# Optimization experiments

Hardware: AMD Instinct MI355X
Metric: run time of the kernel (lower is better)

## Reference

```python
import jax, jax.numpy as jnp
import numpy as np
import math

B, IMG, P, C_IN = 32, 32, 2, 4
D, TED, L, H = 768, 256, 12, 12
GRID = IMG // P            # 16
N = GRID * GRID            # 256 patches
HD = D // H                # 64 head dim
MLP_H = 4 * D
RPD = 2 * GRID - 1         # 31 relative-position table side


def _ln(x, w, b, eps=1e-6):
    m = x.mean(-1, keepdims=True)
    v = ((x - m) ** 2).mean(-1, keepdims=True)
    return (x - m) * jax.lax.rsqrt(v + eps) * w + b


def _rel_idx():
    c = jnp.arange(GRID)
    ch, cw = jnp.meshgrid(c, c, indexing='ij')
    cf = jnp.stack([ch.reshape(-1), cw.reshape(-1)])          # [2, N]
    rel = cf[:, :, None] - cf[:, None, :] + (GRID - 1)        # [2, N, N] in [0, 2*GRID-2]
    return rel[0], rel[1]


def setup_inputs() -> dict:
    key = jax.random.key(0)
    ks = iter(jax.random.split(key, 64))
    def nrm(shape, s=0.02):
        return jax.random.normal(next(ks), shape, jnp.float32) * s
    z = lambda *s: jnp.zeros(s, jnp.float32)
    o = lambda *s: jnp.ones(s, jnp.float32)
    return dict(
        x=jax.random.normal(next(ks), (B, C_IN, IMG, IMG), jnp.float32),
        t=jax.random.uniform(next(ks), (B,), jnp.float32) * 1000.0,
        patch_w=nrm((D, C_IN, P, P), 0.5), patch_b=z(D),
        pos_embed=nrm((1, N, D)),
        t_w1=nrm((TED, D)), t_b1=z(D), t_w2=nrm((D, D)), t_b2=z(D),
        norm1_w=o(L, D), norm1_b=z(L, D),
        wqs=nrm((L, D, D)), bqs=z(L, D), wqt=nrm((L, D, D)), bqt=z(L, D),
        wks=nrm((L, D, D)), bks=z(L, D), wkt=nrm((L, D, D)), bkt=z(L, D),
        wvs=nrm((L, D, D)), bvs=z(L, D), wvt=nrm((L, D, D)), bvt=z(L, D),
        attn_proj_w=nrm((L, D, D)), attn_proj_b=z(L, D),
        rpb=nrm((L, RPD, RPD, H)),
        norm2_w=o(L, D), norm2_b=z(L, D),
        mlp_w1=nrm((L, D, MLP_H)), mlp_b1=z(L, MLP_H),
        mlp_w2=nrm((L, MLP_H, D)), mlp_b2=z(L, D),
        norm_w=o(D), norm_b=z(D),
        dec_w=nrm((D, P * P * C_IN)), dec_b=z(P * P * C_IN),
    )


def reference(x, t, patch_w, patch_b, pos_embed, t_w1, t_b1, t_w2, t_b2,
              norm1_w, norm1_b, wqs, bqs, wqt, bqt, wks, bks, wkt, bkt,
              wvs, bvs, wvt, bvt, attn_proj_w, attn_proj_b, rpb,
              norm2_w, norm2_b, mlp_w1, mlp_b1, mlp_w2, mlp_b2,
              norm_w, norm_b, dec_w, dec_b):
    Bn = x.shape[0]
    # patch embed: stride==kernel Conv2d as reshape + einsum -> [B, N, D]
    xr = x.reshape(Bn, C_IN, GRID, P, GRID, P)
    x_s = jnp.einsum('bcipjq,ecpq->bije', xr, patch_w).reshape(Bn, N, D) + patch_b
    x_s = x_s + pos_embed
    # sinusoidal time embedding + MLP -> [B, D]
    half = TED // 2
    freq = jnp.exp(jnp.arange(half, dtype=jnp.float32) * (-math.log(10000.0) / (half - 1)))
    emb = t[:, None] * freq[None, :]
    emb = jnp.concatenate([jnp.sin(emb), jnp.cos(emb)], axis=-1)
    x_t = jax.nn.silu(emb @ t_w1 + t_b1) @ t_w2 + t_b2
    ih, iw = _rel_idx()
    scale = HD ** -0.5
    for l in range(L):
        h = _ln(x_s, norm1_w[l], norm1_b[l])
        q = h @ wqs[l] + bqs[l] + (x_t @ wqt[l] + bqt[l])[:, None, :]
        k = h @ wks[l] + bks[l] + (x_t @ wkt[l] + bkt[l])[:, None, :]
        v = h @ wvs[l] + bvs[l] + (x_t @ wvt[l] + bvt[l])[:, None, :]
        q = q.reshape(Bn, N, H, HD)
        k = k.reshape(Bn, N, H, HD)
        v = v.reshape(Bn, N, H, HD)
        bias = rpb[l][ih, iw]                                  # gather: [N, N, H]
        attn = jnp.einsum('bnhd,bmhd->bhnm', q, k) * scale + bias.transpose(2, 0, 1)[None]
        attn = jax.nn.softmax(attn, axis=-1)
        o_ = jnp.einsum('bhnm,bmhd->bnhd', attn, v).reshape(Bn, N, D)
        x_s = x_s + (o_ @ attn_proj_w[l] + attn_proj_b[l])
        h2 = _ln(x_s, norm2_w[l], norm2_b[l])
        x_s = x_s + (jax.nn.silu(h2 @ mlp_w1[l] + mlp_b1[l]) @ mlp_w2[l] + mlp_b2[l])
    x_s = _ln(x_s, norm_w, norm_b)
    x_s = x_s @ dec_w + dec_b                                  # [B, N, P*P*C]
    # unpatchify -> [B, C, IMG, IMG]
    xo = x_s.reshape(Bn, GRID, GRID, C_IN, P, P).transpose(0, 3, 1, 4, 2, 5)
    return xo.reshape(Bn, C_IN, GRID * P, GRID * P)
```

## Files before the change

kernel.cpp:

```cpp
#include <hip/hip_runtime.h>
#include <hip/hip_bf16.h>

typedef __attribute__((ext_vector_type(8))) short short8;
typedef __attribute__((ext_vector_type(4))) short s16x4;
typedef __attribute__((ext_vector_type(4))) float f32x4;
typedef __hip_bfloat16 bf16;

#define AS1 __attribute__((address_space(1)))
#define AS3 __attribute__((address_space(3)))

__device__ __forceinline__ float b2f(short u) {
  union { unsigned int i; float f; } x;
  x.i = ((unsigned int)(unsigned short)u) << 16;
  return x.f;
}
__device__ __forceinline__ short f2bs(float f) {
  bf16 t = __float2bfloat16(f);
  return *reinterpret_cast<short*>(&t);
}

__device__ __forceinline__ void gld_lds16(const void* g, void* lds) {
  __builtin_amdgcn_global_load_lds((const AS1 unsigned int*)g,
                                   (AS3 unsigned int*)lds, 16, 0, 0);
}

__global__ void transpose_conv(const float* __restrict__ src, bf16* __restrict__ dst,
                               int R, int C, int row_off, long long layer_stride) {
  __shared__ float t[32][33];
  int l = blockIdx.z;
  int r0 = blockIdx.y * 32;
  int c0 = blockIdx.x * 32;
  int tx = threadIdx.x & 31, ty = threadIdx.x >> 5;
  const float* s = src + (size_t)l * R * C;
#pragma unroll
  for (int i = 0; i < 4; ++i)
    t[ty + i * 8][tx] = s[(size_t)(r0 + ty + i * 8) * C + c0 + tx];
  __syncthreads();
  bf16* d = dst + (size_t)l * layer_stride;
#pragma unroll
  for (int i = 0; i < 4; ++i) {
    int n = c0 + ty + i * 8, k = r0 + tx;
    d[(size_t)(row_off + n) * R + k] = __float2bfloat16(t[tx][ty + i * 8]);
  }
}

__global__ void dec_transpose(const float* __restrict__ dw, bf16* __restrict__ dwT) {
  int idx = blockIdx.x * 256 + threadIdx.x;
  if (idx >= 12288) return;
  int k = idx % 768, j = idx / 768;
  dwT[j * 768 + k] = __float2bfloat16(dw[k * 16 + j]);
}

__global__ void patch_embed(const float* __restrict__ x, const float* __restrict__ pw,
                            const float* __restrict__ pb, const float* __restrict__ pos,
                            float* __restrict__ xs) {
  int idx = blockIdx.x * 256 + threadIdx.x;
  int d = idx % 768;
  int n = (idx / 768) & 255;
  int b = idx / (768 * 256);
  int gi = n >> 4, gj = n & 15;
  float acc = pb[d];
#pragma unroll
  for (int c = 0; c < 4; ++c)
#pragma unroll
    for (int p = 0; p < 2; ++p)
#pragma unroll
      for (int q = 0; q < 2; ++q)
        acc += x[((b * 4 + c) * 32 + gi * 2 + p) * 32 + gj * 2 + q] *
               pw[((d * 4 + c) * 2 + p) * 2 + q];
  xs[idx] = acc + pos[n * 768 + d];
}

__global__ void temb_kernel(const float* __restrict__ t, float* __restrict__ emb) {
  int b = blockIdx.x;
  int i = threadIdx.x;
  float f = __expf((float)i * (-logf(10000.f) / 127.f));
  float e = t[b] * f;
  emb[b * 256 + i] = sinf(e);
  emb[b * 256 + 128 + i] = cosf(e);
}

template <int MODE>
__global__ void smallmm_red(const float* __restrict__ in, const float* __restrict__ w,
                            const float* __restrict__ bias, void* __restrict__ out, int K) {
  int tid = threadIdx.x;
  int s = tid & 7, o = blockIdx.x * 32 + (tid >> 3);
  int d = o % 768, b = o / 768;
  int Ks = K >> 3, k0 = s * Ks;
  const float* ir = in + b * K + k0;
  const float* wr = w + (size_t)k0 * 768 + d;
  float a = 0.f;
  for (int i = 0; i < Ks; ++i) a += ir[i] * wr[(size_t)i * 768];
  a += __shfl_xor(a, 1);
  a += __shfl_xor(a, 2);
  a += __shfl_xor(a, 4);
  if (s == 0) {
    a += bias[d];
    if (MODE == 0) {
      a = a / (1.f + __expf(-a));
      ((float*)out)[o] = a;
    } else {
      ((bf16*)out)[o] = __float2bfloat16(a);
    }
  }
}

__global__ void build_btab_frag(const float* __restrict__ rpb, bf16* __restrict__ btf) {
  int idx = blockIdx.x * 256 + threadIdx.x;
  int t = idx & 65535;
  int lh = idx >> 16;
  int h = lh % 12, l = lh / 12;
  int r = t & 3; t >>= 2;
  int lane = t & 63; t >>= 6;
  int i = t & 3; t >>= 2;
  int w = t & 3; t >>= 2;
  int jb = t & 1; t >>= 1;
  int hc = t & 7;
  int q = w * 64 + i * 16 + (lane & 15);
  int k = hc * 32 + jb * 16 + (lane >> 4) * 4 + r;
  int ih = (q >> 4) - (k >> 4) + 15;
  int iw = (q & 15) - (k & 15) + 15;
  btf[idx] = __float2bfloat16(8.0f * rpb[((l * 31 + ih) * 31 + iw) * 12 + h]);
}

__global__ __launch_bounds__(256) void ln_bf16_kernel(const float* __restrict__ x,
                                                      const float* __restrict__ w,
                                                      const float* __restrict__ b,
                                                      bf16* __restrict__ out) {
  int row = blockIdx.x * 4 + (threadIdx.x >> 6);
  int lane = threadIdx.x & 63;
  const float* xr = x + (size_t)row * 768;
  float v[12];
  float s = 0.f, s2 = 0.f;
#pragma unroll
  for (int k = 0; k < 12; ++k) {
    v[k] = xr[lane + k * 64];
    s += v[k];
    s2 += v[k] * v[k];
  }
#pragma unroll
  for (int off = 32; off; off >>= 1) {
    s += __shfl_xor(s, off);
    s2 += __shfl_xor(s2, off);
  }
  float m = s * (1.f / 768.f);
  float var = s2 * (1.f / 768.f) - m * m;
  float r = rsqrtf(var + 1e-6f);
  bf16* orow = out + (size_t)row * 768;
#pragma unroll
  for (int k = 0; k < 12; ++k) {
    int c = lane + k * 64;
    orow[c] = __float2bfloat16((v[k] - m) * r * w[c] + b[c]);
  }
}

template <int EPI>
__global__ __launch_bounds__(256) void gemm128(
    const bf16* __restrict__ A, int lda, const bf16* __restrict__ BT, int ldb, int K,
    const float* __restrict__ p0, const float* __restrict__ p1,
    const float* __restrict__ p2, const float* __restrict__ p3,
    const float* __restrict__ p4, const float* __restrict__ p5,
    const float* __restrict__ resid, float* __restrict__ outF,
    bf16* __restrict__ outB, int ldc) {
  __shared__ __align__(16) char lds[49152];
  const int tid = threadIdx.x;
  const int wid = tid >> 6, lane = tid & 63;
  const int wr = wid >> 1, wc = wid & 1;
  const int nwg = gridDim.x * gridDim.y;
  const int bid = blockIdx.y * gridDim.x + blockIdx.x;
  const int swzb = (bid & 7) * (nwg >> 3) + (bid >> 3);
  const int m0 = (swzb / gridDim.x) * 128, n0 = (swzb % gridDim.x) * 128;
  const int l16 = lane & 15, lq = lane >> 4;

  f32x4 acc[4][4];
#pragma unroll
  for (int i = 0; i < 4; ++i)
#pragma unroll
    for (int j = 0; j < 4; ++j) acc[i][j] = f32x4{0.f, 0.f, 0.f, 0.f};

  const int arow = tid >> 2;
  const int aslot = (tid & 3) ^ ((tid >> 4) & 3);
  const bf16* gA = A + (size_t)(m0 + arow) * lda + aslot * 8;
  const bf16* gB = BT + (size_t)(n0 + arow) * ldb + aslot * 8;
  const unsigned offw = (unsigned)__builtin_amdgcn_readfirstlane((tid & ~63) * 16);

  const int NT = K >> 5;
  auto stage = [&](int t, int buf) {
    char* pA = lds + buf * 16384;
    char* pB = pA + 8192;
    const int k = t * 32;
#pragma unroll
    for (int e = 0; e < 2; ++e) {
      gld_lds16(gA + (size_t)(e * 64) * lda + k, pA + e * 4096 + offw);
      gld_lds16(gB + (size_t)(e * 64) * ldb + k, pB + e * 4096 + offw);
    }
  };

  stage(0, 0);
  if (NT > 1) stage(1, 1);
  int cb = 0;
  for (int t = 0; t < NT; ++t) {
    if (t + 2 < NT) {
      int sb = cb + 2; if (sb >= 3) sb -= 3;
      stage(t + 2, sb);
      asm volatile("s_waitcnt vmcnt(8)" ::: "memory");
    } else if (t + 1 < NT) {
      asm volatile("s_waitcnt vmcnt(4)" ::: "memory");
    } else {
      asm volatile("s_waitcnt vmcnt(0)" ::: "memory");
    }
    __builtin_amdgcn_s_barrier();
    char* pA = lds + cb * 16384;
    char* pB = pA + 8192;
    short8 af[4], bfr[4];
    const unsigned ko = ((unsigned)(lq * 16)) ^ ((unsigned)(l16 >> 2) << 4);
#pragma unroll
    for (int i = 0; i < 4; ++i) {
      af[i]  = *(const short8*)(pA + (wr * 64 + i * 16 + l16) * 64 + ko);
      bfr[i] = *(const short8*)(pB + (wc * 64 + i * 16 + l16) * 64 + ko);
    }
#pragma unroll
    for (int i = 0; i < 4; ++i)
#pragma unroll
      for (int j = 0; j < 4; ++j)
        acc[i][j] = __builtin_amdgcn_mfma_f32_16x16x32_bf16(af[i], bfr[j], acc[i][j], 0, 0, 0);
    __builtin_amdgcn_s_barrier();
    cb = (cb == 2) ? 0 : cb + 1;
  }

#pragma unroll
  for (int i = 0; i < 4; ++i) {
#pragma unroll
    for (int j = 0; j < 4; ++j) {
#pragma unroll
      for (int r = 0; r < 4; ++r) {
        int row = m0 + wr * 64 + i * 16 + lq * 4 + r;
        int col = n0 + wc * 64 + j * 16 + l16;
        float v = acc[i][j][r];
        if constexpr (EPI == 0) {
          int s = col / 768, d = col % 768;
          int b = row >> 8;
          const float* bs = (s == 0) ? p0 : (s == 1) ? p1 : p2;
          const float* ts = (s == 0) ? p3 : (s == 1) ? p4 : p5;
          v += bs[d] + ts[b * 768 + d];
          outB[(size_t)row * ldc + col] = __float2bfloat16(v);
        } else if constexpr (EPI == 1) {
          v += p0[col] + resid[(size_t)row * ldc + col];
          outF[(size_t)row * ldc + col] = v;
        } else if constexpr (EPI == 2) {
          v += p0[col];
          v = v / (1.f + __expf(-v));
          outB[(size_t)row * ldc + col] = __float2bfloat16(v);
        } else if constexpr (EPI == 3) {
          if (row < 32) {
            int l = col / 2304;
            int r2c = col - l * 2304;
            int s = r2c / 768, d = r2c - s * 768;
            const float* bs = (s == 0) ? p0 : (s == 1) ? p1 : p2;
            v += bs[l * 768 + d];
            outF[(size_t)((l * 3 + s) * 32 + row) * 768 + d] = v;
          }
        } else {
          if (col < 16) {
            v += p0[col];
            int b = row >> 8, n = row & 255;
            int gi = n >> 4, gj = n & 15;
            int c = col >> 2, pp = (col >> 1) & 1, qq = col & 1;
            outF[((b * 4 + c) * 32 + gi * 2 + pp) * 32 + gj * 2 + qq] = v;
          }
        }
      }
    }
  }
}

__global__ __launch_bounds__(256) void attn_mfma(const bf16* __restrict__ qkv,
                                                 const bf16* __restrict__ btf,
                                                 bf16* __restrict__ obuf) {
  __shared__ __align__(16) char lds[65536];
  const int tid = threadIdx.x;
  const int wave = tid >> 6, lane = tid & 63;
  const int l16 = lane & 15, lq = lane >> 4;
  const int b = blockIdx.x / 12, h = blockIdx.x % 12;
  const bf16* qb = qkv + (size_t)b * 256 * 2304;

  {
    const short8* vrow = (const short8*)(qb + (size_t)tid * 2304 + 1536 + h * 64);
    short8 vv[8];
#pragma unroll
    for (int c = 0; c < 8; ++c) vv[c] = vrow[c];
#pragma unroll
    for (int c = 0; c < 8; ++c)
#pragma unroll
      for (int e = 0; e < 8; ++e) {
        int d = c * 8 + e;
        unsigned off = (unsigned)(d * 512 + tid * 2) ^ ((unsigned)(d & 7) << 4);
        *(short*)(lds + off) = vv[c][e];
      }
  }
  short8 qf[4][2];
#pragma unroll
  for (int i = 0; i < 4; ++i)
#pragma unroll
    for (int ks = 0; ks < 2; ++ks)
      qf[i][ks] = *(const short8*)(qb + (size_t)(wave * 64 + i * 16 + l16) * 2304 +
                                   h * 64 + ks * 32 + lq * 8);
  __syncthreads();

  f32x4 oacc[4][4];
#pragma unroll
  for (int i = 0; i < 4; ++i)
#pragma unroll
    for (int j = 0; j < 4; ++j) oacc[i][j] = f32x4{0.f, 0.f, 0.f, 0.f};
  float lp[4] = {0.f, 0.f, 0.f, 0.f};
  const bf16* bl = btf + (size_t)h * 65536 + lane * 4;
  const unsigned swzv = ((unsigned)(l16 & 7)) << 4;
  const unsigned swzp = ((unsigned)(l16 & 3)) << 4;

  for (int hc = 0; hc < 8; ++hc) {
    short8 kf[2][2];
#pragma unroll
    for (int jb = 0; jb < 2; ++jb) {
      const bf16* kr = qb + (size_t)(hc * 32 + jb * 16 + l16) * 2304 + 768 + h * 64 + lq * 8;
      kf[jb][0] = *(const short8*)(kr);
      kf[jb][1] = *(const short8*)(kr + 32);
    }
    f32x4 sacc[4][2];
#pragma unroll
    for (int i = 0; i < 4; ++i)
#pragma unroll
      for (int jb = 0; jb < 2; ++jb) {
        s16x4 bv = *(const s16x4*)(bl + ((size_t)((hc * 2 + jb) * 16 + wave * 4 + i) << 8));
        sacc[i][jb] = f32x4{b2f(bv[0]), b2f(bv[1]), b2f(bv[2]), b2f(bv[3])};
      }
#pragma unroll
    for (int jb = 0; jb < 2; ++jb)
#pragma unroll
      for (int i = 0; i < 4; ++i) {
        sacc[i][jb] = __builtin_amdgcn_mfma_f32_16x16x32_bf16(kf[jb][0], qf[i][0], sacc[i][jb], 0, 0, 0);
        sacc[i][jb] = __builtin_amdgcn_mfma_f32_16x16x32_bf16(kf[jb][1], qf[i][1], sacc[i][jb], 0, 0, 0);
      }
    char* Pw = lds + 32768 + (hc & 1) * 16384 + wave * 4096;
#pragma unroll
    for (int i = 0; i < 4; ++i)
#pragma unroll
      for (int jb = 0; jb < 2; ++jb) {
        float p0 = __expf(sacc[i][jb][0] * 0.125f);
        float p1 = __expf(sacc[i][jb][1] * 0.125f);
        float p2 = __expf(sacc[i][jb][2] * 0.125f);
        float p3 = __expf(sacc[i][jb][3] * 0.125f);
        lp[i] += (p0 + p1) + (p2 + p3);
        s16x4 pk = {f2bs(p0), f2bs(p1), f2bs(p2), f2bs(p3)};
        *(s16x4*)(Pw + (i * 16 + l16) * 64 + (((unsigned)(jb * 32 + lq * 8)) ^ swzp)) = pk;
      }
    asm volatile("s_waitcnt lgkmcnt(0)" ::: "memory");
    __builtin_amdgcn_sched_barrier(0);
    short8 pa[4], vb[4];
#pragma unroll
    for (int i = 0; i < 4; ++i)
      pa[i] = *(const short8*)(Pw + (i * 16 + l16) * 64 + (((unsigned)(lq * 16)) ^ swzp));
#pragma unroll
    for (int dj = 0; dj < 4; ++dj)
      vb[dj] = *(const short8*)(lds + (dj * 16 + l16) * 512 +
                                (((unsigned)(hc * 64 + lq * 16)) ^ swzv));
#pragma unroll
    for (int i = 0; i < 4; ++i)
#pragma unroll
      for (int dj = 0; dj < 4; ++dj)
        oacc[i][dj] = __builtin_amdgcn_mfma_f32_16x16x32_bf16(pa[i], vb[dj], oacc[i][dj], 0, 0, 0);
  }

#pragma unroll
  for (int i = 0; i < 4; ++i) {
    float l = lp[i];
    l += __shfl_xor(l, 16);
    l += __shfl_xor(l, 32);
#pragma unroll
    for (int r = 0; r < 4; ++r) {
      float linv = 1.f / __shfl(l, lq * 4 + r);
      int grow = b * 256 + wave * 64 + i * 16 + lq * 4 + r;
#pragma unroll
      for (int dj = 0; dj < 4; ++dj)
        obuf[(size_t)grow * 768 + h * 64 + dj * 16 + l16] =
            __float2bfloat16(oacc[i][dj][r] * linv);
    }
  }
}

extern "C" void kernel_launch(void* const* d_in, const int* in_sizes, int n_in,
                              void* d_out, int out_size, void* d_ws, size_t ws_size,
                              hipStream_t stream) {
  (void)in_sizes; (void)n_in; (void)out_size; (void)ws_size;
  const float* x       = (const float*)d_in[0];
  const float* t_in    = (const float*)d_in[1];
  const float* patch_w = (const float*)d_in[2];
  const float* patch_b = (const float*)d_in[3];
  const float* pos     = (const float*)d_in[4];
  const float* t_w1    = (const float*)d_in[5];
  const float* t_b1    = (const float*)d_in[6];
  const float* t_w2    = (const float*)d_in[7];
  const float* t_b2    = (const float*)d_in[8];
  const float* norm1_w = (const float*)d_in[9];
  const float* norm1_b = (const float*)d_in[10];
  const float* wqs     = (const float*)d_in[11];
  const float* bqs     = (const float*)d_in[12];
  const float* wqt     = (const float*)d_in[13];
  const float* bqt     = (const float*)d_in[14];
  const float* wks     = (const float*)d_in[15];
  const float* bks     = (const float*)d_in[16];
  const float* wkt     = (const float*)d_in[17];
  const float* bkt     = (const float*)d_in[18];
  const float* wvs     = (const float*)d_in[19];
  const float* bvs     = (const float*)d_in[20];
  const float* wvt     = (const float*)d_in[21];
  const float* bvt     = (const float*)d_in[22];
  const float* projw   = (const float*)d_in[23];
  const float* projb   = (const float*)d_in[24];
  const float* rpb     = (const float*)d_in[25];
  const float* norm2_w = (const float*)d_in[26];
  const float* norm2_b = (const float*)d_in[27];
  const float* mlp_w1  = (const float*)d_in[28];
  const float* mlp_b1  = (const float*)d_in[29];
  const float* mlp_w2  = (const float*)d_in[30];
  const float* mlp_b2  = (const float*)d_in[31];
  const float* norm_w  = (const float*)d_in[32];
  const float* norm_b  = (const float*)d_in[33];
  const float* dec_w   = (const float*)d_in[34];
  const float* dec_b   = (const float*)d_in[35];

  char* ws = (char*)d_ws;
  size_t off = 0;
  auto alloc = [&](size_t bytes) -> void* {
    void* p = ws + off;
    off += (bytes + 255) & ~(size_t)255;
    return p;
  };
  bf16* wqkvT = (bf16*)alloc(12ull * 2304 * 768 * 2);
  bf16* projT = (bf16*)alloc(12ull * 768 * 768 * 2);
  bf16* mlp1T = (bf16*)alloc(12ull * 3072 * 768 * 2);
  bf16* mlp2T = (bf16*)alloc(12ull * 768 * 3072 * 2);
  bf16* wtT   = (bf16*)alloc(12ull * 2304 * 768 * 2);
  float* xs   = (float*)alloc(8192ull * 768 * 4);
  bf16* hbuf  = (bf16*)alloc(8192ull * 768 * 2);
  bf16* qkvb  = (bf16*)alloc(8192ull * 2304 * 2);
  bf16* obuf  = (bf16*)alloc(8192ull * 768 * 2);
  bf16* btabf = (bf16*)alloc(12ull * 12 * 256 * 256 * 2);
  float* ttok = (float*)alloc(12ull * 3 * 32 * 768 * 4);
  bf16* xtb   = (bf16*)alloc(128ull * 768 * 2);
  bf16* dwT   = (bf16*)alloc(128ull * 768 * 2);
  float* emb  = (float*)alloc(32ull * 256 * 4);
  float* h1   = (float*)alloc(32ull * 768 * 4);
  bf16* hmlp  = qkvb;

  hipMemsetAsync(xtb, 0, 128ull * 768 * 2, stream);
  hipMemsetAsync(dwT, 0, 128ull * 768 * 2, stream);

  transpose_conv<<<dim3(24, 24, 12), 256, 0, stream>>>(wqs, wqkvT, 768, 768, 0, 2304ll * 768);
  transpose_conv<<<dim3(24, 24, 12), 256, 0, stream>>>(wks, wqkvT, 768, 768, 768, 2304ll * 768);
  transpose_conv<<<dim3(24, 24, 12), 256, 0, stream>>>(wvs, wqkvT, 768, 768, 1536, 2304ll * 768);
  transpose_conv<<<dim3(24, 24, 12), 256, 0, stream>>>(projw, projT, 768, 768, 0, 768ll * 768);
  transpose_conv<<<dim3(96, 24, 12), 256, 0, stream>>>(mlp_w1, mlp1T, 768, 3072, 0, 3072ll * 768);
  transpose_conv<<<dim3(24, 96, 12), 256, 0, stream>>>(mlp_w2, mlp2T, 3072, 768, 0, 768ll * 3072);
  transpose_conv<<<dim3(24, 24, 12), 256, 0, stream>>>(wqt, wtT, 768, 768, 0, 2304ll * 768);
  transpose_conv<<<dim3(24, 24, 12), 256, 0, stream>>>(wkt, wtT, 768, 768, 768, 2304ll * 768);
  transpose_conv<<<dim3(24, 24, 12), 256, 0, stream>>>(wvt, wtT, 768, 768, 1536, 2304ll * 768);
  dec_transpose<<<48, 256, 0, stream>>>(dec_w, dwT);
  build_btab_frag<<<36864, 256, 0, stream>>>(rpb, btabf);

  temb_kernel<<<32, 128, 0, stream>>>(t_in, emb);
  smallmm_red<0><<<768, 256, 0, stream>>>(emb, t_w1, t_b1, h1, 256);
  smallmm_red<1><<<768, 256, 0, stream>>>(h1, t_w2, t_b2, xtb, 768);
  gemm128<3><<<dim3(216, 1), 256, 0, stream>>>(
      xtb, 768, wtT, 768, 768, bqt, bkt, bvt, nullptr, nullptr, nullptr,
      nullptr, ttok, nullptr, 0);

  patch_embed<<<24576, 256, 0, stream>>>(x, patch_w, patch_b, pos, xs);

  for (int l = 0; l < 12; ++l) {
    ln_bf16_kernel<<<2048, 256, 0, stream>>>(xs, norm1_w + l * 768, norm1_b + l * 768, hbuf);
    gemm128<0><<<dim3(18, 64), 256, 0, stream>>>(
        hbuf, 768, wqkvT + (size_t)l * 2304 * 768, 768, 768,
        bqs + l * 768, bks + l * 768, bvs + l * 768,
        ttok + (size_t)(l * 3 + 0) * 32 * 768,
        ttok + (size_t)(l * 3 + 1) * 32 * 768,
        ttok + (size_t)(l * 3 + 2) * 32 * 768,
        nullptr, nullptr, qkvb, 2304);
    attn_mfma<<<384, 256, 0, stream>>>(qkvb, btabf + (size_t)l * 12 * 65536, obuf);
    gemm128<1><<<dim3(6, 64), 256, 0, stream>>>(
        obuf, 768, projT + (size_t)l * 768 * 768, 768, 768,
        projb + l * 768, nullptr, nullptr, nullptr, nullptr, nullptr,
        xs, xs, nullptr, 768);
    ln_bf16_kernel<<<2048, 256, 0, stream>>>(xs, norm2_w + l * 768, norm2_b + l * 768, hbuf);
    gemm128<2><<<dim3(24, 64), 256, 0, stream>>>(
        hbuf, 768, mlp1T + (size_t)l * 3072 * 768, 768, 768,
        mlp_b1 + l * 3072, nullptr, nullptr, nullptr, nullptr, nullptr,
        nullptr, nullptr, hmlp, 3072);
    gemm128<1><<<dim3(6, 64), 256, 0, stream>>>(
        hmlp, 3072, mlp2T + (size_t)l * 768 * 3072, 3072, 3072,
        mlp_b2 + l * 768, nullptr, nullptr, nullptr, nullptr, nullptr,
        xs, xs, nullptr, 768);
  }
  ln_bf16_kernel<<<2048, 256, 0, stream>>>(xs, norm_w, norm_b, hbuf);
  gemm128<4><<<dim3(1, 64), 256, 0, stream>>>(
      hbuf, 768, dwT, 768, 768, dec_b, nullptr, nullptr, nullptr, nullptr, nullptr,
      nullptr, (float*)d_out, nullptr, 0);
}
```

Before: 2.901 ms.

## Add 256-row ping-pong GEMM with split-N phases for transformer layer GEMMs

Introduces a new 512-thread GEMM kernel with 256xBN tiles (BN=256 or 128). It double-buffers A and B in LDS and splits each k-step into two MFMA phases over halves of N, interleaving B-fragment reloads and next-tile loads with s_setprio and barriers. All four per-layer GEMMs (QKV, proj, MLP1, MLP2) now use it instead of the 128x128 kernel. The aim is more data reuse per LDS byte and better overlap of loads with MFMA. The LDS swizzle in the old kernel also changes, and its now-unused epilogues are dropped. Risks are register pressure from the larger accumulator and fewer workgroups for the N=768 GEMMs (192 blocks).

```diff
diff --git a/kernel.cpp b/kernel.cpp
--- a/kernel.cpp
+++ b/kernel.cpp
@@ -154,6 +154,139 @@
   }
 }
 
+template <int EPI, int NJ>
+__global__ __launch_bounds__(512, 2) void gemm256ph(
+    const bf16* __restrict__ A, int lda, const bf16* __restrict__ BT, int ldb, int K,
+    const float* __restrict__ p0, const float* __restrict__ p1,
+    const float* __restrict__ p2, const float* __restrict__ p3,
+    const float* __restrict__ p4, const float* __restrict__ p5,
+    const float* __restrict__ resid, float* __restrict__ outF,
+    bf16* __restrict__ outB, int ldc) {
+  constexpr int BN = NJ * 64;
+  constexpr int BB = BN * 64;
+  __shared__ __align__(16) char lds[32768 + 2 * BB];
+  const int tid = threadIdx.x;
+  const int wid = tid >> 6, lane = tid & 63;
+  const int wm = wid >> 2, wn = wid & 3;
+  const int l16 = lane & 15, lq = lane >> 4;
+
+  const int nwg = gridDim.x * gridDim.y;
+  int bid = blockIdx.y * gridDim.x + blockIdx.x;
+  bid = (bid & 7) * (nwg >> 3) + (bid >> 3);
+  const int m0 = (bid / gridDim.x) * 256, n0 = (bid % gridDim.x) * BN;
+
+  f32x4 acc[8][NJ];
+#pragma unroll
+  for (int i = 0; i < 8; ++i)
+#pragma unroll
+    for (int j = 0; j < NJ; ++j) acc[i][j] = f32x4{0.f, 0.f, 0.f, 0.f};
+
+  const int sr = tid >> 2;
+  const int ss = (tid & 3) ^ ((tid >> 3) & 3);
+  const bf16* gA = A + (size_t)(m0 + sr) * lda + ss * 8;
+  const bf16* gB = BT + (size_t)(n0 + sr) * ldb + ss * 8;
+  const unsigned offw = (unsigned)__builtin_amdgcn_readfirstlane((tid & ~63) * 16);
+
+  auto stageA = [&](int t) {
+    char* d = lds + (t & 1) * 16384;
+    const int kb = t * 32;
+    gld_lds16(gA + kb, d + offw);
+    gld_lds16(gA + (size_t)128 * lda + kb, d + 8192 + offw);
+  };
+  auto stageB = [&](int t) {
+    char* d = lds + 32768 + (t & 1) * BB;
+    const int kb = t * 32;
+    gld_lds16(gB + kb, d + offw);
+    if constexpr (NJ == 4) gld_lds16(gB + (size_t)128 * ldb + kb, d + 8192 + offw);
+  };
+
+  const int NT = K >> 5;
+  stageA(0); stageB(0); stageA(1);
+  asm volatile("s_waitcnt vmcnt(2)" ::: "memory");
+  __builtin_amdgcn_s_barrier();
+
+  const unsigned ko0 = ((unsigned)(lq * 16)) ^ ((((unsigned)l16 >> 1) & 3) << 4);
+  const int rA0 = wm * 128 + l16;
+  const int rB0 = wn * (NJ * 16) + l16;
+
+  for (int t = 0; t < NT; ++t) {
+    char* pa = lds + (t & 1) * 16384;
+    char* pb = lds + 32768 + (t & 1) * BB;
+    short8 afr[8], bfr[NJ / 2];
+#pragma unroll
+    for (int mi = 0; mi < 8; ++mi)
+      afr[mi] = *(const short8*)(pa + (rA0 + mi * 16) * 64 + ko0);
+#pragma unroll
+    for (int jj = 0; jj < NJ / 2; ++jj)
+      bfr[jj] = *(const short8*)(pb + (rB0 + jj * 16) * 64 + ko0);
+    if (t + 1 < NT) stageB(t + 1);
+    __builtin_amdgcn_sched_barrier(0);
+    __builtin_amdgcn_s_barrier();
+    asm volatile("s_waitcnt lgkmcnt(0)" ::: "memory");
+    __builtin_amdgcn_sched_barrier(0);
+    __builtin_amdgcn_s_setprio(1);
+#pragma unroll
+    for (int mi = 0; mi < 8; ++mi)
+#pragma unroll
+      for (int jj = 0; jj < NJ / 2; ++jj)
+        acc[mi][jj] = __builtin_amdgcn_mfma_f32_16x16x32_bf16(afr[mi], bfr[jj], acc[mi][jj], 0, 0, 0);
+    __builtin_amdgcn_s_setprio(0);
+    __builtin_amdgcn_sched_barrier(0);
+    __builtin_amdgcn_s_barrier();
+#pragma unroll
+    for (int jj = 0; jj < NJ / 2; ++jj)
+      bfr[jj] = *(const short8*)(pb + (rB0 + (NJ / 2 + jj) * 16) * 64 + ko0);
+    if (t + 2 < NT) {
+      stageA(t + 2);
+      asm volatile("s_waitcnt vmcnt(2)" ::: "memory");
+    } else {
+      asm volatile("s_waitcnt vmcnt(0)" ::: "memory");
+    }
+    __builtin_amdgcn_sched_barrier(0);
+    __builtin_amdgcn_s_barrier();
+    asm volatile("s_waitcnt lgkmcnt(0)" ::: "memory");
+    __builtin_amdgcn_sched_barrier(0);
+    __builtin_amdgcn_s_setprio(1);
+#pragma unroll
+    for (int mi = 0; mi < 8; ++mi)
+#pragma unroll
+      for (int jj = 0; jj < NJ / 2; ++jj)
+        acc[mi][NJ / 2 + jj] =
+            __builtin_amdgcn_mfma_f32_16x16x32_bf16(afr[mi], bfr[jj], acc[mi][NJ / 2 + jj], 0, 0, 0);
+    __builtin_amdgcn_s_setprio(0);
+    __builtin_amdgcn_sched_barrier(0);
+    __builtin_amdgcn_s_barrier();
+  }
+
+#pragma unroll
+  for (int mi = 0; mi < 8; ++mi) {
+#pragma unroll
+    for (int nj = 0; nj < NJ; ++nj) {
+#pragma unroll
+      for (int r = 0; r < 4; ++r) {
+        int row = m0 + wm * 128 + mi * 16 + lq * 4 + r;
+        int col = n0 + wn * (NJ * 16) + nj * 16 + l16;
+        float v = acc[mi][nj][r];
+        if constexpr (EPI == 0) {
+          int s = col / 768, d = col % 768;
+          int b = row >> 8;
+          const float* bs = (s == 0) ? p0 : (s == 1) ? p1 : p2;
+          const float* ts = (s == 0) ? p3 : (s == 1) ? p4 : p5;
+          v += bs[d] + ts[b * 768 + d];
+          outB[(size_t)row * ldc + col] = __float2bfloat16(v);
+        } else if constexpr (EPI == 1) {
+          v += p0[col] + resid[(size_t)row * ldc + col];
+          outF[(size_t)row * ldc + col] = v;
+        } else {
+          v += p0[col];
+          v = v / (1.f + __expf(-v));
+          outB[(size_t)row * ldc + col] = __float2bfloat16(v);
+        }
+      }
+    }
+  }
+}
+
 template <int EPI>
 __global__ __launch_bounds__(256) void gemm128(
     const bf16* __restrict__ A, int lda, const bf16* __restrict__ BT, int ldb, int K,
@@ -179,7 +312,7 @@
     for (int j = 0; j < 4; ++j) acc[i][j] = f32x4{0.f, 0.f, 0.f, 0.f};
 
   const int arow = tid >> 2;
-  const int aslot = (tid & 3) ^ ((tid >> 4) & 3);
+  const int aslot = (tid & 3) ^ ((tid >> 3) & 3);
   const bf16* gA = A + (size_t)(m0 + arow) * lda + aslot * 8;
   const bf16* gB = BT + (size_t)(n0 + arow) * ldb + aslot * 8;
   const unsigned offw = (unsigned)__builtin_amdgcn_readfirstlane((tid & ~63) * 16);
@@ -213,7 +346,7 @@
     char* pA = lds + cb * 16384;
     char* pB = pA + 8192;
     short8 af[4], bfr[4];
-    const unsigned ko = ((unsigned)(lq * 16)) ^ ((unsigned)(l16 >> 2) << 4);
+    const unsigned ko = ((unsigned)(lq * 16)) ^ ((((unsigned)l16 >> 1) & 3) << 4);
 #pragma unroll
     for (int i = 0; i < 4; ++i) {
       af[i]  = *(const short8*)(pA + (wr * 64 + i * 16 + l16) * 64 + ko);
@@ -237,21 +370,7 @@
         int row = m0 + wr * 64 + i * 16 + lq * 4 + r;
         int col = n0 + wc * 64 + j * 16 + l16;
         float v = acc[i][j][r];
-        if constexpr (EPI == 0) {
-          int s = col / 768, d = col % 768;
-          int b = row >> 8;
-          const float* bs = (s == 0) ? p0 : (s == 1) ? p1 : p2;
-          const float* ts = (s == 0) ? p3 : (s == 1) ? p4 : p5;
-          v += bs[d] + ts[b * 768 + d];
-          outB[(size_t)row * ldc + col] = __float2bfloat16(v);
-        } else if constexpr (EPI == 1) {
-          v += p0[col] + resid[(size_t)row * ldc + col];
-          outF[(size_t)row * ldc + col] = v;
-        } else if constexpr (EPI == 2) {
-          v += p0[col];
-          v = v / (1.f + __expf(-v));
-          outB[(size_t)row * ldc + col] = __float2bfloat16(v);
-        } else if constexpr (EPI == 3) {
+        if constexpr (EPI == 3) {
           if (row < 32) {
             int l = col / 2304;
             int r2c = col - l * 2304;
@@ -478,7 +597,7 @@
 
   for (int l = 0; l < 12; ++l) {
     ln_bf16_kernel<<<2048, 256, 0, stream>>>(xs, norm1_w + l * 768, norm1_b + l * 768, hbuf);
-    gemm128<0><<<dim3(18, 64), 256, 0, stream>>>(
+    gemm256ph<0, 4><<<dim3(9, 32), 512, 0, stream>>>(
         hbuf, 768, wqkvT + (size_t)l * 2304 * 768, 768, 768,
         bqs + l * 768, bks + l * 768, bvs + l * 768,
         ttok + (size_t)(l * 3 + 0) * 32 * 768,
@@ -486,16 +605,16 @@
         ttok + (size_t)(l * 3 + 2) * 32 * 768,
         nullptr, nullptr, qkvb, 2304);
     attn_mfma<<<384, 256, 0, stream>>>(qkvb, btabf + (size_t)l * 12 * 65536, obuf);
-    gemm128<1><<<dim3(6, 64), 256, 0, stream>>>(
+    gemm256ph<1, 2><<<dim3(6, 32), 512, 0, stream>>>(
         obuf, 768, projT + (size_t)l * 768 * 768, 768, 768,
         projb + l * 768, nullptr, nullptr, nullptr, nullptr, nullptr,
         xs, xs, nullptr, 768);
     ln_bf16_kernel<<<2048, 256, 0, stream>>>(xs, norm2_w + l * 768, norm2_b + l * 768, hbuf);
-    gemm128<2><<<dim3(24, 64), 256, 0, stream>>>(
+    gemm256ph<2, 4><<<dim3(12, 32), 512, 0, stream>>>(
         hbuf, 768, mlp1T + (size_t)l * 3072 * 768, 768, 768,
         mlp_b1 + l * 3072, nullptr, nullptr, nullptr, nullptr, nullptr,
         nullptr, nullptr, hmlp, 3072);
-    gemm128<1><<<dim3(6, 64), 256, 0, stream>>>(
+    gemm256ph<1, 2><<<dim3(6, 32), 512, 0, stream>>>(
         hmlp, 3072, mlp2T + (size_t)l * 768 * 3072, 3072, 3072,
         mlp_b2 + l * 768, nullptr, nullptr, nullptr, nullptr, nullptr,
         xs, xs, nullptr, 768);
```

New measurement: 3.454 ms. 19.1% more time.
